# Kernel optimization log

Hardware: AMD Instinct MI355X
Metric: run time of the kernel (lower is better)

The kernel has to match this reference:

```python
import jax, jax.numpy as jnp
import numpy as np

FIRST_THRESHOLD = 0.5  # quantile_list[0][0]


def setup_inputs() -> dict:
    key = jax.random.key(0)
    k1, k2, k3 = jax.random.split(key, 3)
    L, H, B, N, E = 8192, 4096, 2, 2, 2
    x = jax.random.normal(k1, (L, H), dtype=jnp.float32)
    weights = jax.random.uniform(k2, (B, N), dtype=jnp.float32)  # dynamic objective weights in [0,1)
    W = 0.02 * jax.random.normal(k3, (E, H), dtype=jnp.float32)  # CustomLinearv0 weight (init 0, perturbed)
    b = jnp.ones((E,), dtype=jnp.float32)                         # CustomLinearv0 bias (init 1)
    return {"x": x, "weights": weights, "W": W, "b": b}


def reference(x, weights, W, b):
    L, H = x.shape
    B, N = weights.shape            # N = num_obj = 2
    E = W.shape[0]                  # num_experts = N
    K = N + 1                       # num_router = 3
    ft = FIRST_THRESHOLD
    st = 1.0 - ft

    # repeat weights so each batch row covers its seq_len chunk: [L, N]
    extra = jnp.repeat(weights, L // B, axis=0)

    # WeightingRouter: vectorized per-row threshold branch -> [L, K]
    hs = extra[:, 0]
    zeros = jnp.zeros_like(hs)
    hi = jnp.stack([(hs - ft) / st, zeros, (1.0 - hs) / st], axis=1)
    lo = jnp.stack([zeros, (ft - hs) / ft, hs / ft], axis=1)
    rr_logits = jnp.where((hs >= ft)[:, None], hi, lo)  # [L, K]

    # step1: stack per-router expert logits -> [K, L, E]
    # first N routers are constant one-hots; last is normalized linear
    onehot = jnp.broadcast_to(jnp.eye(N, E, dtype=x.dtype)[:, None, :], (N, L, E))
    lin = x @ W.T + b                                    # [L, E]
    lin = lin / jnp.sum(lin, axis=-1, keepdims=True)
    all_router_logits = jnp.concatenate([onehot, lin[None]], axis=0)  # [K, L, E]

    # step2: combine -> [L, E]
    out = jnp.einsum('kle,lk->le', all_router_logits, rr_logits)
    return out
```

## Files before the change

kernel.cpp:

```cpp
#include <hip/hip_runtime.h>


#define L_DIM 8192
#define H_DIM 4096

typedef float f32x4 __attribute__((ext_vector_type(4)));

__global__ __launch_bounds__(256) void router_kernel(
    const float* __restrict__ x,
    const float* __restrict__ weights,
    const float* __restrict__ W,
    const float* __restrict__ b,
    float* __restrict__ out)
{
    __shared__ float sW0[H_DIM];
    __shared__ float sW1[H_DIM];

    for (int i = threadIdx.x; i < H_DIM / 4; i += 256) {
        ((f32x4*)sW0)[i] = ((const f32x4*)W)[i];
        ((f32x4*)sW1)[i] = ((const f32x4*)(W + H_DIM))[i];
    }
    __syncthreads();

    const int wave = threadIdx.x >> 6;
    const int lane = threadIdx.x & 63;
    const int row0 = blockIdx.x * 8 + wave * 2;

    const f32x4* xr0 = (const f32x4*)(x + (size_t)row0 * H_DIM);
    const f32x4* xr1 = (const f32x4*)(x + (size_t)(row0 + 1) * H_DIM);
    const f32x4* w0v = (const f32x4*)sW0;
    const f32x4* w1v = (const f32x4*)sW1;

    float a00 = 0.f, a01 = 0.f;
    float a10 = 0.f, a11 = 0.f;

    #pragma unroll
    for (int j = 0; j < H_DIM / 256; ++j) {
        const int idx = j * 64 + lane;
        const f32x4 xa = __builtin_nontemporal_load(&xr0[idx]);
        const f32x4 xb = __builtin_nontemporal_load(&xr1[idx]);
        const f32x4 wa = w0v[idx];
        const f32x4 wb = w1v[idx];
        a00 += xa.x * wa.x + xa.y * wa.y + xa.z * wa.z + xa.w * wa.w;
        a01 += xa.x * wb.x + xa.y * wb.y + xa.z * wb.z + xa.w * wb.w;
        a10 += xb.x * wa.x + xb.y * wa.y + xb.z * wa.z + xb.w * wa.w;
        a11 += xb.x * wb.x + xb.y * wb.y + xb.z * wb.z + xb.w * wb.w;
    }

    #pragma unroll
    for (int off = 32; off > 0; off >>= 1) {
        a00 += __shfl_down(a00, off, 64);
        a01 += __shfl_down(a01, off, 64);
        a10 += __shfl_down(a10, off, 64);
        a11 += __shfl_down(a11, off, 64);
    }

    if (lane == 0) {
        const float b0 = b[0], b1 = b[1];
        float4 o;
        {
            const float lin0 = a00 + b0, lin1 = a01 + b1;
            const float inv = 1.0f / (lin0 + lin1);
            const float hs = weights[(row0 >> 12) * 2];
            float r0, r1, r2;
            if (hs >= 0.5f) { r0 = (hs - 0.5f) * 2.f; r1 = 0.f; r2 = (1.f - hs) * 2.f; }
            else            { r0 = 0.f; r1 = (0.5f - hs) * 2.f; r2 = hs * 2.f; }
            o.x = r0 + r2 * (lin0 * inv);
            o.y = r1 + r2 * (lin1 * inv);
        }
        {
            const float lin0 = a10 + b0, lin1 = a11 + b1;
            const float inv = 1.0f / (lin0 + lin1);
            const float hs = weights[((row0 + 1) >> 12) * 2];
            float r0, r1, r2;
            if (hs >= 0.5f) { r0 = (hs - 0.5f) * 2.f; r1 = 0.f; r2 = (1.f - hs) * 2.f; }
            else            { r0 = 0.f; r1 = (0.5f - hs) * 2.f; r2 = hs * 2.f; }
            o.z = r0 + r2 * (lin0 * inv);
            o.w = r1 + r2 * (lin1 * inv);
        }
        *(float4*)(out + row0 * 2) = o;
    }
}

extern "C" void kernel_launch(void* const* d_in, const int* in_sizes, int n_in,
                              void* d_out, int out_size, void* d_ws, size_t ws_size,
                              hipStream_t stream) {
    const float* x       = (const float*)d_in[0];
    const float* weights = (const float*)d_in[1];
    const float* W       = (const float*)d_in[2];
    const float* b       = (const float*)d_in[3];
    float* out           = (float*)d_out;

    router_kernel<<<L_DIM / 8, 256, 0, stream>>>(x, weights, W, b, out);
}
```

Measured before the change: 184.2 us.

## Split hidden dim across waves, keep W slice in registers, reduce via LDS

Each wave now handles a quarter of the hidden dimension for all 8 rows of the block and keeps its W slice in registers. This drops the 32KB shared-memory staging of W and the LDS reads in the inner loop. Partial sums are reduced across waves through a small shared buffer. The 32KB of LDS per block is freed, which should allow higher occupancy. The cost is more register pressure from the accumulators and W fragments, plus an extra block-level sync and cross-wave reduction.

```diff
diff --git a/kernel.cpp b/kernel.cpp
--- a/kernel.cpp
+++ b/kernel.cpp
@@ -6,79 +6,90 @@
 
 typedef float f32x4 __attribute__((ext_vector_type(4)));
 
-__global__ __launch_bounds__(256) void router_kernel(
+__global__ __launch_bounds__(256, 4) void router_kernel(
     const float* __restrict__ x,
     const float* __restrict__ weights,
     const float* __restrict__ W,
     const float* __restrict__ b,
     float* __restrict__ out)
 {
-    __shared__ float sW0[H_DIM];
-    __shared__ float sW1[H_DIM];
-
-    for (int i = threadIdx.x; i < H_DIM / 4; i += 256) {
-        ((f32x4*)sW0)[i] = ((const f32x4*)W)[i];
-        ((f32x4*)sW1)[i] = ((const f32x4*)(W + H_DIM))[i];
-    }
-    __syncthreads();
+    __shared__ float sRed[4][8][2];
 
     const int wave = threadIdx.x >> 6;
     const int lane = threadIdx.x & 63;
-    const int row0 = blockIdx.x * 8 + wave * 2;
+    const int row_base = blockIdx.x * 8;
 
-    const f32x4* xr0 = (const f32x4*)(x + (size_t)row0 * H_DIM);
-    const f32x4* xr1 = (const f32x4*)(x + (size_t)(row0 + 1) * H_DIM);
-    const f32x4* w0v = (const f32x4*)sW0;
-    const f32x4* w1v = (const f32x4*)sW1;
+    const int qoff = wave * 256;
+    const f32x4* w0q = (const f32x4*)W + qoff;
+    const f32x4* w1q = (const f32x4*)(W + H_DIM) + qoff;
 
-    float a00 = 0.f, a01 = 0.f;
-    float a10 = 0.f, a11 = 0.f;
+    f32x4 wr0[4], wr1[4];
+    #pragma unroll
+    for (int j = 0; j < 4; ++j) {
+        wr0[j] = w0q[j * 64 + lane];
+        wr1[j] = w1q[j * 64 + lane];
+    }
+
+    float acc0[8], acc1[8];
+    #pragma unroll
+    for (int r = 0; r < 8; ++r) { acc0[r] = 0.f; acc1[r] = 0.f; }
+
+    const f32x4* xbase = (const f32x4*)(x + (size_t)row_base * H_DIM) + qoff;
 
     #pragma unroll
-    for (int j = 0; j < H_DIM / 256; ++j) {
-        const int idx = j * 64 + lane;
-        const f32x4 xa = __builtin_nontemporal_load(&xr0[idx]);
-        const f32x4 xb = __builtin_nontemporal_load(&xr1[idx]);
-        const f32x4 wa = w0v[idx];
-        const f32x4 wb = w1v[idx];
-        a00 += xa.x * wa.x + xa.y * wa.y + xa.z * wa.z + xa.w * wa.w;
-        a01 += xa.x * wb.x + xa.y * wb.y + xa.z * wb.z + xa.w * wb.w;
-        a10 += xb.x * wa.x + xb.y * wa.y + xb.z * wa.z + xb.w * wa.w;
-        a11 += xb.x * wb.x + xb.y * wb.y + xb.z * wb.z + xb.w * wb.w;
+    for (int r = 0; r < 8; ++r) {
+        const f32x4* xr = xbase + (size_t)r * (H_DIM / 4);
+        #pragma unroll
+        for (int j = 0; j < 4; ++j) {
+            const f32x4 xv = __builtin_nontemporal_load(&xr[j * 64 + lane]);
+            acc0[r] += xv.x * wr0[j].x + xv.y * wr0[j].y + xv.z * wr0[j].z + xv.w * wr0[j].w;
+            acc1[r] += xv.x * wr1[j].x + xv.y * wr1[j].y + xv.z * wr1[j].z + xv.w * wr1[j].w;
+        }
     }
 
     #pragma unroll
     for (int off = 32; off > 0; off >>= 1) {
-        a00 += __shfl_down(a00, off, 64);
-        a01 += __shfl_down(a01, off, 64);
-        a10 += __shfl_down(a10, off, 64);
-        a11 += __shfl_down(a11, off, 64);
+        #pragma unroll
+        for (int r = 0; r < 8; ++r) {
+            acc0[r] += __shfl_down(acc0[r], off, 64);
+            acc1[r] += __shfl_down(acc1[r], off, 64);
+        }
     }
 
     if (lane == 0) {
+        #pragma unroll
+        for (int r = 0; r < 8; ++r) {
+            sRed[wave][r][0] = acc0[r];
+            sRed[wave][r][1] = acc1[r];
+        }
+    }
+    __syncthreads();
+
+    if (threadIdx.x < 4) {
+        const int r0 = threadIdx.x * 2;
         const float b0 = b[0], b1 = b[1];
+        const float hs = weights[(blockIdx.x >> 9) * 2];
+        float c0, c1, c2;
+        if (hs >= 0.5f) { c0 = (hs - 0.5f) * 2.f; c1 = 0.f; c2 = (1.f - hs) * 2.f; }
+        else            { c0 = 0.f; c1 = (0.5f - hs) * 2.f; c2 = hs * 2.f; }
+
         float4 o;
         {
-            const float lin0 = a00 + b0, lin1 = a01 + b1;
+            const float lin0 = sRed[0][r0][0] + sRed[1][r0][0] + sRed[2][r0][0] + sRed[3][r0][0] + b0;
+            const float lin1 = sRed[0][r0][1] + sRed[1][r0][1] + sRed[2][r0][1] + sRed[3][r0][1] + b1;
             const float inv = 1.0f / (lin0 + lin1);
-            const float hs = weights[(row0 >> 12) * 2];
-            float r0, r1, r2;
-            if (hs >= 0.5f) { r0 = (hs - 0.5f) * 2.f; r1 = 0.f; r2 = (1.f - hs) * 2.f; }
-            else            { r0 = 0.f; r1 = (0.5f - hs) * 2.f; r2 = hs * 2.f; }
-            o.x = r0 + r2 * (lin0 * inv);
-            o.y = r1 + r2 * (lin1 * inv);
+            o.x = c0 + c2 * (lin0 * inv);
+            o.y = c1 + c2 * (lin1 * inv);
         }
         {
-            const float lin0 = a10 + b0, lin1 = a11 + b1;
+            const int r1 = r0 + 1;
+            const float lin0 = sRed[0][r1][0] + sRed[1][r1][0] + sRed[2][r1][0] + sRed[3][r1][0] + b0;
+            const float lin1 = sRed[0][r1][1] + sRed[1][r1][1] + sRed[2][r1][1] + sRed[3][r1][1] + b1;
             const float inv = 1.0f / (lin0 + lin1);
-            const float hs = weights[((row0 + 1) >> 12) * 2];
-            float r0, r1, r2;
-            if (hs >= 0.5f) { r0 = (hs - 0.5f) * 2.f; r1 = 0.f; r2 = (1.f - hs) * 2.f; }
-            else            { r0 = 0.f; r1 = (0.5f - hs) * 2.f; r2 = hs * 2.f; }
-            o.z = r0 + r2 * (lin0 * inv);
-            o.w = r1 + r2 * (lin1 * inv);
+            o.z = c0 + c2 * (lin0 * inv);
+            o.w = c1 + c2 * (lin1 * inv);
         }
-        *(float4*)(out + row0 * 2) = o;
+        *(float4*)(out + (size_t)(row_base + r0) * 2) = o;
     }
 }
 
```

After: 184.6 us. Within noise of the previous version (+0.2%).
